# Kernel tuning notes

Measured on AMD Instinct MI355X. Metric: run time of the kernel, lower is better.

The kernel has to match this reference:

```python
import jax, jax.numpy as jnp
import numpy as np
from jax import lax

D = 1024   # bond dimension
d = 32     # physical dimension (alphabet size)
F = 1024   # n_features (chain length)


def setup_inputs() -> dict:
    key = jax.random.key(0)
    k1, k2, k3, k4 = jax.random.split(key, 4)
    x = jax.random.randint(k1, (F,), 0, d)
    # scale uniform cores by 2/D so the 1024-step product chain stays O(1)
    core = jax.random.uniform(k2, (d, D, D), dtype=jnp.float32) * (2.0 / D)
    left_boundary = jax.random.uniform(k3, (D,), dtype=jnp.float32)
    right_boundary = jax.random.uniform(k4, (D,), dtype=jnp.float32)
    return {"x": x, "core": core, "left_boundary": left_boundary,
            "right_boundary": right_boundary}


def reference(x, core, left_boundary, right_boundary):
    # Faithful to TN._contract_at: sequential chain of vector-matrix products
    # v <- v @ core[x[i]] for i in range(n_features), then v . right_boundary.
    # The original's repeat_interleave of `core` is a mathematical no-op; we
    # gather core[x[i]] inside the scan step instead of materializing F copies.
    def step(v, xi):
        return v @ core[xi], None  # (D,) @ (D, D) -> (D,)

    v, _ = lax.scan(step, left_boundary, x)
    return jnp.dot(v, right_boundary)  # scalar unnormalized probability
```

## Files before the change

kernel.cpp:

```cpp
#include <hip/hip_runtime.h>
#include <stdint.h>

#define TN_D 1024
#define TN_F 1024
#define SENT32 0xAAAAAAAAu
#define NBLK 64
#define CPB 16

typedef _Float16 half8_t __attribute__((ext_vector_type(8)));

__global__ __launch_bounds__(256) void tn_transpose(const float* __restrict__ core,
                                                    _Float16* __restrict__ coreT) {
    __shared__ float tile[64][65];
    const int s = blockIdx.z;
    const size_t base = (size_t)s * TN_D * TN_D;
    const int j0 = blockIdx.x * 64;
    const int i0 = blockIdx.y * 64;
    const int tx = threadIdx.x;
    const int ty = threadIdx.y;
#pragma unroll
    for (int r = 0; r < 4; ++r) {
        const int ii = ty + 16 * r;
        const float4 v = *(const float4*)&core[base + (size_t)(i0 + ii) * TN_D + j0 + 4 * tx];
        tile[ii][4 * tx + 0] = v.x; tile[ii][4 * tx + 1] = v.y;
        tile[ii][4 * tx + 2] = v.z; tile[ii][4 * tx + 3] = v.w;
    }
    __syncthreads();
#pragma unroll
    for (int r = 0; r < 4; ++r) {
        const int jj = ty + 16 * r;
        _Float16 h4[4];
        h4[0] = (_Float16)tile[4 * tx + 0][jj];
        h4[1] = (_Float16)tile[4 * tx + 1][jj];
        h4[2] = (_Float16)tile[4 * tx + 2][jj];
        h4[3] = (_Float16)tile[4 * tx + 3][jj];
        *(uint64_t*)&coreT[base + (size_t)(j0 + jj) * TN_D + i0 + 4 * tx] = *(uint64_t*)h4;
    }
}

__device__ __forceinline__ float poll1(const uint32_t* p) {
    uint32_t u = __hip_atomic_load(p, __ATOMIC_RELAXED, __HIP_MEMORY_SCOPE_AGENT);
    while (u == SENT32)
        u = __hip_atomic_load(p, __ATOMIC_RELAXED, __HIP_MEMORY_SCOPE_AGENT);
    return __uint_as_float(u);
}

__device__ __forceinline__ float dot8h(float4 a, float4 b, half8_t h) {
    return a.x * (float)h[0] + a.y * (float)h[1] + a.z * (float)h[2] + a.w * (float)h[3] +
           b.x * (float)h[4] + b.y * (float)h[5] + b.z * (float)h[6] + b.w * (float)h[7];
}

__global__ __launch_bounds__(1024, 1) void tn_chain_f16(const int* __restrict__ x,
                                                        const _Float16* __restrict__ mat,
                                                        const float* __restrict__ left,
                                                        const float* __restrict__ right,
                                                        float* __restrict__ vg,
                                                        float* __restrict__ out) {
    __shared__ float lv[2][TN_D];
    __shared__ int xs[TN_F];
    volatile __shared__ uint32_t redv[CPB];
    __shared__ float red2[CPB];

    const int tid = threadIdx.x;
    const int w = tid >> 6;
    const int l = tid & 63;
    const int j = blockIdx.x * CPB + w;

    xs[tid] = x[tid];
    if (tid < CPB) redv[tid] = SENT32;
    __syncthreads();

    half8_t A0, A1, B0, B1;
    {
        const half8_t* cp = (const half8_t*)(mat + ((size_t)xs[0] * TN_D + j) * TN_D);
        A0 = cp[l]; A1 = cp[l + 64];
    }

    for (int t = 0; t < TN_F; t += 2) {
        const int s1 = xs[(t + 1 < TN_F) ? t + 1 : TN_F - 1];
        const int s2 = xs[(t + 2 < TN_F) ? t + 2 : TN_F - 1];

        if (t == 0) lv[0][tid] = left[tid];
        else        lv[0][tid] = poll1((const uint32_t*)vg + (size_t)(t - 1) * TN_D + tid);
        __syncthreads();
        {
            const half8_t* cp = (const half8_t*)(mat + ((size_t)s1 * TN_D + j) * TN_D);
            B0 = cp[l]; B1 = cp[l + 64];
        }
        {
            const float4* vv = (const float4*)lv[0];
            float acc = dot8h(vv[2 * l], vv[2 * l + 1], A0) +
                        dot8h(vv[2 * l + 128], vv[2 * l + 129], A1);
#pragma unroll
            for (int off = 32; off; off >>= 1) acc += __shfl_down(acc, off, 64);
            if (l == 0) {
                __asm__ volatile("" ::: "memory");
                redv[w] = __float_as_uint(acc);
            }
            if (w == 0 && l < CPB) {
                uint32_t u = redv[l];
                while (u == SENT32) u = redv[l];
                redv[l] = SENT32;
                __asm__ volatile("" ::: "memory");
                __hip_atomic_store((uint32_t*)vg + (size_t)t * TN_D + blockIdx.x * CPB + l,
                                   u, __ATOMIC_RELAXED, __HIP_MEMORY_SCOPE_AGENT);
            }
        }

        lv[1][tid] = poll1((const uint32_t*)vg + (size_t)t * TN_D + tid);
        __syncthreads();
        {
            const half8_t* cp = (const half8_t*)(mat + ((size_t)s2 * TN_D + j) * TN_D);
            A0 = cp[l]; A1 = cp[l + 64];
        }
        {
            const float4* vv = (const float4*)lv[1];
            float acc = dot8h(vv[2 * l], vv[2 * l + 1], B0) +
                        dot8h(vv[2 * l + 128], vv[2 * l + 129], B1);
#pragma unroll
            for (int off = 32; off; off >>= 1) acc += __shfl_down(acc, off, 64);
            if (l == 0) {
                __asm__ volatile("" ::: "memory");
                redv[w] = __float_as_uint(acc);
            }
            if (w == 0 && l < CPB) {
                uint32_t u = redv[l];
                while (u == SENT32) u = redv[l];
                redv[l] = SENT32;
                __asm__ volatile("" ::: "memory");
                __hip_atomic_store((uint32_t*)vg + (size_t)(t + 1) * TN_D + blockIdx.x * CPB + l,
                                   u, __ATOMIC_RELAXED, __HIP_MEMORY_SCOPE_AGENT);
            }
        }
    }

    if (blockIdx.x == 0) {
        float v = poll1((const uint32_t*)vg + (size_t)(TN_F - 1) * TN_D + tid);
        float p = v * right[tid];
#pragma unroll
        for (int off = 32; off; off >>= 1) p += __shfl_down(p, off, 64);
        if (l == 0) red2[w] = p;
        __syncthreads();
        if (tid == 0) {
            float s = 0.f;
#pragma unroll
            for (int k = 0; k < CPB; ++k) s += red2[k];
            out[0] = s;
        }
    }
}

__device__ __forceinline__ float4 poll4(const uint32_t* vp) {
    const unsigned long long* p = (const unsigned long long*)vp;
    unsigned long long a = __hip_atomic_load(p, __ATOMIC_RELAXED, __HIP_MEMORY_SCOPE_AGENT);
    unsigned long long b = __hip_atomic_load(p + 1, __ATOMIC_RELAXED, __HIP_MEMORY_SCOPE_AGENT);
    while ((uint32_t)a == SENT32 || (uint32_t)(a >> 32) == SENT32)
        a = __hip_atomic_load(p, __ATOMIC_RELAXED, __HIP_MEMORY_SCOPE_AGENT);
    while ((uint32_t)b == SENT32 || (uint32_t)(b >> 32) == SENT32)
        b = __hip_atomic_load(p + 1, __ATOMIC_RELAXED, __HIP_MEMORY_SCOPE_AGENT);
    return make_float4(__uint_as_float((uint32_t)a), __uint_as_float((uint32_t)(a >> 32)),
                       __uint_as_float((uint32_t)b), __uint_as_float((uint32_t)(b >> 32)));
}

__global__ __launch_bounds__(256, 1) void tn_chain_f32(const int* __restrict__ x,
                                                       const float* __restrict__ mat,
                                                       const float* __restrict__ left,
                                                       const float* __restrict__ right,
                                                       float* __restrict__ vg,
                                                       float* __restrict__ out) {
    __shared__ float4 lv[2][TN_D / 4];
    __shared__ float red[4];
    const int tid = threadIdx.x;
    const int w = tid >> 6;
    const int l = tid & 63;
    const int j = blockIdx.x * 4 + w;

    for (int t = 0; t < TN_F; ++t) {
        if (t == 0) lv[0][tid] = ((const float4*)left)[tid];
        else lv[t & 1][tid] = poll4((const uint32_t*)vg + (size_t)(t - 1) * TN_D + 4 * tid);
        __syncthreads();
        const float* mp = mat + (size_t)x[t] * TN_D * TN_D + j;
        const float4* vv = lv[t & 1];
        float acc = 0.f;
#pragma unroll
        for (int k = 0; k < 4; ++k) {
            const int i = 4 * l + 256 * k;
            const float4 v = vv[l + 64 * k];
            acc += v.x * mp[(size_t)i * TN_D] + v.y * mp[(size_t)(i + 1) * TN_D] +
                   v.z * mp[(size_t)(i + 2) * TN_D] + v.w * mp[(size_t)(i + 3) * TN_D];
        }
#pragma unroll
        for (int off = 32; off; off >>= 1) acc += __shfl_down(acc, off, 64);
        if (l == 0)
            __hip_atomic_store((uint32_t*)vg + (size_t)t * TN_D + j, __float_as_uint(acc),
                               __ATOMIC_RELAXED, __HIP_MEMORY_SCOPE_AGENT);
    }
    if (blockIdx.x == 0) {
        float4 v = poll4((const uint32_t*)vg + (size_t)(TN_F - 1) * TN_D + 4 * tid);
        const float4 r4 = ((const float4*)right)[tid];
        float p = v.x * r4.x + v.y * r4.y + v.z * r4.z + v.w * r4.w;
#pragma unroll
        for (int off = 32; off; off >>= 1) p += __shfl_down(p, off, 64);
        if (l == 0) red[w] = p;
        __syncthreads();
        if (tid == 0) out[0] = red[0] + red[1] + red[2] + red[3];
    }
}

extern "C" void kernel_launch(void* const* d_in, const int* in_sizes, int n_in,
                              void* d_out, int out_size, void* d_ws, size_t ws_size,
                              hipStream_t stream) {
    const int* x = (const int*)d_in[0];
    const float* core = (const float*)d_in[1];
    const float* left = (const float*)d_in[2];
    const float* right = (const float*)d_in[3];
    float* out = (float*)d_out;

    const int nsym = in_sizes[1] / (TN_D * TN_D);
    const size_t coreTBytes = (size_t)in_sizes[1] * sizeof(_Float16);
    const size_t vbufBytes = (size_t)TN_F * TN_D * sizeof(float);

    if (ws_size >= coreTBytes + vbufBytes) {
        _Float16* coreT = (_Float16*)d_ws;
        float* vg = (float*)((char*)d_ws + coreTBytes);
        hipMemsetAsync(vg, 0xAA, vbufBytes, stream);
        tn_transpose<<<dim3(16, 16, nsym), dim3(16, 16), 0, stream>>>(core, coreT);
        tn_chain_f16<<<NBLK, 1024, 0, stream>>>(x, coreT, left, right, vg, out);
    } else {
        float* vg = (float*)d_ws;
        hipMemsetAsync(vg, 0xAA, vbufBytes, stream);
        tn_chain_f32<<<256, 256, 0, stream>>>(x, core, left, right, vg, out);
    }
}
```

Before: 1.834 ms.

## Fuse two chain steps per grid barrier using split-K atomic accumulation

Each block now computes 16 entries of the intermediate vector from the full input, then multiplies those partials by the matching 16 rows of the next core and atomically adds into the output vector. Two chain steps therefore share one grid-wide synchronisation, halving the barriers. Blocks signal completion through a per-round counter instead of polling sentinel values per element. The cost is 64-way float atomic contention per element each round and a non-deterministic summation order.

```diff
diff --git a/kernel.cpp b/kernel.cpp
--- a/kernel.cpp
+++ b/kernel.cpp
@@ -6,8 +6,11 @@
 #define SENT32 0xAAAAAAAAu
 #define NBLK 64
 #define CPB 16
+#define NR (TN_F / 2)
+#define CNT_STRIDE 16
 
 typedef _Float16 half8_t __attribute__((ext_vector_type(8)));
+typedef _Float16 half4_t __attribute__((ext_vector_type(4)));
 
 __global__ __launch_bounds__(256) void tn_transpose(const float* __restrict__ core,
                                                     _Float16* __restrict__ coreT) {
@@ -38,114 +41,110 @@
     }
 }
 
-__device__ __forceinline__ float poll1(const uint32_t* p) {
-    uint32_t u = __hip_atomic_load(p, __ATOMIC_RELAXED, __HIP_MEMORY_SCOPE_AGENT);
-    while (u == SENT32)
-        u = __hip_atomic_load(p, __ATOMIC_RELAXED, __HIP_MEMORY_SCOPE_AGENT);
-    return __uint_as_float(u);
-}
-
-__device__ __forceinline__ float dot8h(float4 a, float4 b, half8_t h) {
-    return a.x * (float)h[0] + a.y * (float)h[1] + a.z * (float)h[2] + a.w * (float)h[3] +
-           b.x * (float)h[4] + b.y * (float)h[5] + b.z * (float)h[6] + b.w * (float)h[7];
-}
-
-__global__ __launch_bounds__(1024, 1) void tn_chain_f16(const int* __restrict__ x,
-                                                        const _Float16* __restrict__ mat,
-                                                        const float* __restrict__ left,
-                                                        const float* __restrict__ right,
-                                                        float* __restrict__ vg,
-                                                        float* __restrict__ out) {
-    __shared__ float lv[2][TN_D];
+__device__ __forceinline__ float dot4h(float4 a, half4_t h) {
+    return a.x * (float)h[0] + a.y * (float)h[1] + a.z * (float)h[2] + a.w * (float)h[3];
+}
+
+__device__ __forceinline__ void poll_cnt(const uint32_t* cp) {
+    uint32_t a = __hip_atomic_load(cp, __ATOMIC_RELAXED, __HIP_MEMORY_SCOPE_AGENT);
+    uint32_t b = __hip_atomic_load(cp, __ATOMIC_RELAXED, __HIP_MEMORY_SCOPE_AGENT);
+    while (a < NBLK) {
+        a = b;
+        b = __hip_atomic_load(cp, __ATOMIC_RELAXED, __HIP_MEMORY_SCOPE_AGENT);
+    }
+}
+
+__global__ __launch_bounds__(1024, 1) void tn_chain2(const int* __restrict__ x,
+                                                     const _Float16* __restrict__ mat,
+                                                     const float* __restrict__ left,
+                                                     const float* __restrict__ right,
+                                                     float* __restrict__ acc,
+                                                     uint32_t* __restrict__ cnt,
+                                                     float* __restrict__ out) {
+    __shared__ __align__(16) float lv[TN_D];
+    __shared__ __align__(16) float wl[CPB];
     __shared__ int xs[TN_F];
-    volatile __shared__ uint32_t redv[CPB];
-    __shared__ float red2[CPB];
 
     const int tid = threadIdx.x;
     const int w = tid >> 6;
     const int l = tid & 63;
-    const int j = blockIdx.x * CPB + w;
+    const int b = blockIdx.x;
 
     xs[tid] = x[tid];
-    if (tid < CPB) redv[tid] = SENT32;
     __syncthreads();
 
-    half8_t A0, A1, B0, B1;
+    half4_t A0, A1, A2, A3;
+    half8_t B0, B1;
     {
-        const half8_t* cp = (const half8_t*)(mat + ((size_t)xs[0] * TN_D + j) * TN_D);
-        A0 = cp[l]; A1 = cp[l + 64];
-    }
-
-    for (int t = 0; t < TN_F; t += 2) {
-        const int s1 = xs[(t + 1 < TN_F) ? t + 1 : TN_F - 1];
-        const int s2 = xs[(t + 2 < TN_F) ? t + 2 : TN_F - 1];
-
-        if (t == 0) lv[0][tid] = left[tid];
-        else        lv[0][tid] = poll1((const uint32_t*)vg + (size_t)(t - 1) * TN_D + tid);
-        __syncthreads();
+        const half4_t* cA = (const half4_t*)(mat + ((size_t)xs[0] * TN_D + (CPB * b + w)) * TN_D);
+        A0 = cA[l]; A1 = cA[64 + l]; A2 = cA[128 + l]; A3 = cA[192 + l];
+        const half8_t* cB = (const half8_t*)(mat + ((size_t)xs[1] * TN_D + tid) * TN_D + CPB * b);
+        B0 = cB[0]; B1 = cB[1];
+    }
+
+#pragma unroll 1
+    for (int r = 0; r < NR; ++r) {
+        half4_t nA0, nA1, nA2, nA3;
+        half8_t nB0, nB1;
         {
-            const half8_t* cp = (const half8_t*)(mat + ((size_t)s1 * TN_D + j) * TN_D);
-            B0 = cp[l]; B1 = cp[l + 64];
-        }
-        {
-            const float4* vv = (const float4*)lv[0];
-            float acc = dot8h(vv[2 * l], vv[2 * l + 1], A0) +
-                        dot8h(vv[2 * l + 128], vv[2 * l + 129], A1);
-#pragma unroll
-            for (int off = 32; off; off >>= 1) acc += __shfl_down(acc, off, 64);
-            if (l == 0) {
-                __asm__ volatile("" ::: "memory");
-                redv[w] = __float_as_uint(acc);
-            }
-            if (w == 0 && l < CPB) {
-                uint32_t u = redv[l];
-                while (u == SENT32) u = redv[l];
-                redv[l] = SENT32;
-                __asm__ volatile("" ::: "memory");
-                __hip_atomic_store((uint32_t*)vg + (size_t)t * TN_D + blockIdx.x * CPB + l,
-                                   u, __ATOMIC_RELAXED, __HIP_MEMORY_SCOPE_AGENT);
-            }
-        }
-
-        lv[1][tid] = poll1((const uint32_t*)vg + (size_t)t * TN_D + tid);
-        __syncthreads();
-        {
-            const half8_t* cp = (const half8_t*)(mat + ((size_t)s2 * TN_D + j) * TN_D);
-            A0 = cp[l]; A1 = cp[l + 64];
-        }
-        {
-            const float4* vv = (const float4*)lv[1];
-            float acc = dot8h(vv[2 * l], vv[2 * l + 1], B0) +
-                        dot8h(vv[2 * l + 128], vv[2 * l + 129], B1);
-#pragma unroll
-            for (int off = 32; off; off >>= 1) acc += __shfl_down(acc, off, 64);
-            if (l == 0) {
-                __asm__ volatile("" ::: "memory");
-                redv[w] = __float_as_uint(acc);
-            }
-            if (w == 0 && l < CPB) {
-                uint32_t u = redv[l];
-                while (u == SENT32) u = redv[l];
-                redv[l] = SENT32;
-                __asm__ volatile("" ::: "memory");
-                __hip_atomic_store((uint32_t*)vg + (size_t)(t + 1) * TN_D + blockIdx.x * CPB + l,
-                                   u, __ATOMIC_RELAXED, __HIP_MEMORY_SCOPE_AGENT);
-            }
-        }
-    }
-
-    if (blockIdx.x == 0) {
-        float v = poll1((const uint32_t*)vg + (size_t)(TN_F - 1) * TN_D + tid);
+            const int i2 = 2 * r + 2;
+            const int sA = xs[(i2 < TN_F) ? i2 : 0];
+            const int sB = xs[(i2 + 1 < TN_F) ? i2 + 1 : 0];
+            const half4_t* cA = (const half4_t*)(mat + ((size_t)sA * TN_D + (CPB * b + w)) * TN_D);
+            nA0 = cA[l]; nA1 = cA[64 + l]; nA2 = cA[128 + l]; nA3 = cA[192 + l];
+            const half8_t* cB = (const half8_t*)(mat + ((size_t)sB * TN_D + tid) * TN_D + CPB * b);
+            nB0 = cB[0]; nB1 = cB[1];
+        }
+
+        if (r == 0) {
+            lv[tid] = left[tid];
+        } else {
+            if (w == 0) poll_cnt(cnt + (size_t)(r - 1) * CNT_STRIDE);
+            __syncthreads();
+            lv[tid] = __hip_atomic_load(acc + (size_t)(r - 1) * TN_D + tid,
+                                        __ATOMIC_RELAXED, __HIP_MEMORY_SCOPE_AGENT);
+        }
+        __syncthreads();
+
+        const float4* vv = (const float4*)lv;
+        const float4 v0 = vv[l], v1 = vv[64 + l], v2 = vv[128 + l], v3 = vv[192 + l];
+        float s = dot4h(v0, A0) + dot4h(v1, A1) + dot4h(v2, A2) + dot4h(v3, A3);
+#pragma unroll
+        for (int off = 32; off; off >>= 1) s += __shfl_down(s, off, 64);
+        if (l == 0) wl[w] = s;
+        __syncthreads();
+
+        const float4* w4 = (const float4*)wl;
+        const float4 W0 = w4[0], W1 = w4[1], W2 = w4[2], W3 = w4[3];
+        float p = W0.x * (float)B0[0] + W0.y * (float)B0[1] + W0.z * (float)B0[2] + W0.w * (float)B0[3]
+                + W1.x * (float)B0[4] + W1.y * (float)B0[5] + W1.z * (float)B0[6] + W1.w * (float)B0[7]
+                + W2.x * (float)B1[0] + W2.y * (float)B1[1] + W2.z * (float)B1[2] + W2.w * (float)B1[3]
+                + W3.x * (float)B1[4] + W3.y * (float)B1[5] + W3.z * (float)B1[6] + W3.w * (float)B1[7];
+        atomicAdd(acc + (size_t)r * TN_D + tid, p);
+        __asm__ volatile("s_waitcnt vmcnt(0)" ::: "memory");
+        __syncthreads();
+        if (tid == 0)
+            __hip_atomic_fetch_add(cnt + (size_t)r * CNT_STRIDE, 1u,
+                                   __ATOMIC_RELEASE, __HIP_MEMORY_SCOPE_AGENT);
+
+        A0 = nA0; A1 = nA1; A2 = nA2; A3 = nA3; B0 = nB0; B1 = nB1;
+    }
+
+    if (b == 0) {
+        if (w == 0) poll_cnt(cnt + (size_t)(NR - 1) * CNT_STRIDE);
+        __syncthreads();
+        const float v = __hip_atomic_load(acc + (size_t)(NR - 1) * TN_D + tid,
+                                          __ATOMIC_RELAXED, __HIP_MEMORY_SCOPE_AGENT);
         float p = v * right[tid];
 #pragma unroll
         for (int off = 32; off; off >>= 1) p += __shfl_down(p, off, 64);
-        if (l == 0) red2[w] = p;
+        if (l == 0) wl[w] = p;
         __syncthreads();
         if (tid == 0) {
-            float s = 0.f;
-#pragma unroll
-            for (int k = 0; k < CPB; ++k) s += red2[k];
-            out[0] = s;
+            float t = 0.f;
+#pragma unroll
+            for (int k = 0; k < CPB; ++k) t += wl[k];
+            out[0] = t;
         }
     }
 }
@@ -218,16 +217,19 @@
 
     const int nsym = in_sizes[1] / (TN_D * TN_D);
     const size_t coreTBytes = (size_t)in_sizes[1] * sizeof(_Float16);
-    const size_t vbufBytes = (size_t)TN_F * TN_D * sizeof(float);
-
-    if (ws_size >= coreTBytes + vbufBytes) {
+    const size_t cntBytes = (size_t)NR * CNT_STRIDE * sizeof(uint32_t);
+    const size_t accBytes = (size_t)NR * TN_D * sizeof(float);
+
+    if (ws_size >= coreTBytes + cntBytes + accBytes) {
         _Float16* coreT = (_Float16*)d_ws;
-        float* vg = (float*)((char*)d_ws + coreTBytes);
-        hipMemsetAsync(vg, 0xAA, vbufBytes, stream);
+        uint32_t* cnt = (uint32_t*)((char*)d_ws + coreTBytes);
+        float* acc = (float*)((char*)d_ws + coreTBytes + cntBytes);
+        hipMemsetAsync(cnt, 0, cntBytes + accBytes, stream);
         tn_transpose<<<dim3(16, 16, nsym), dim3(16, 16), 0, stream>>>(core, coreT);
-        tn_chain_f16<<<NBLK, 1024, 0, stream>>>(x, coreT, left, right, vg, out);
+        tn_chain2<<<NBLK, 1024, 0, stream>>>(x, coreT, left, right, acc, cnt, out);
     } else {
         float* vg = (float*)d_ws;
+        const size_t vbufBytes = (size_t)TN_F * TN_D * sizeof(float);
         hipMemsetAsync(vg, 0xAA, vbufBytes, stream);
         tn_chain_f32<<<256, 256, 0, stream>>>(x, core, left, right, vg, out);
     }
```

Measured after the change: 3.392 ms. +85.0%, slower.
